# Kernel tuning notes

Measured on AMD Instinct MI355X. Metric: run time of the kernel, lower is better.

## Reference

```python
import jax, jax.numpy as jnp
import numpy as np

E, L = 16384, 2048          # query events, padded history length
N_NODES, N_COMP = 10000, 20  # Poisson base-rate embedding table
T_MAX = 100.0                # time horizon
MEAN_FEAT, VAR_FEAT = 0.5, 0.25


def setup_inputs() -> dict:
    key = jax.random.key(0)
    ks = jax.random.split(key, 7)
    src = jax.random.randint(ks[0], (E,), 0, N_NODES)
    dst = jax.random.randint(ks[1], (E,), 0, N_NODES)
    t = jax.random.uniform(ks[2], (E,), dtype=jnp.float32) * T_MAX
    x_pad = jax.random.normal(ks[3], (E, L), dtype=jnp.float32)
    # histories sorted in time, as event sequences are
    t_pad = jnp.sort(jax.random.uniform(ks[4], (E, L), dtype=jnp.float32) * T_MAX, axis=1)
    # Poisson base-rate params: per-node embeddings, rate = softplus(<e_src, e_dst>)
    emb_src = jax.random.normal(ks[5], (N_NODES, N_COMP), dtype=jnp.float32) * 0.1
    emb_dst = jax.random.normal(ks[6], (N_NODES, N_COMP), dtype=jnp.float32) * 0.1
    # exponential Hawkes kernel params
    alpha = jnp.float32(0.5)
    beta = jnp.float32(1.0)
    return dict(src=src, dst=dst, t=t, x_pad=x_pad, t_pad=t_pad,
                emb_src=emb_src, emb_dst=emb_dst, alpha=alpha, beta=beta)


def reference(src, dst, t, x_pad, t_pad, emb_src, emb_dst, alpha, beta):
    # base_rate(src, dst): Poisson intensity per event pair
    out = jax.nn.softplus(jnp.einsum('ec,ec->e', emb_src[src], emb_dst[dst]))

    # __get_prev_t_mask / __get_last_t_mask: cumsum-based last-event selection
    mask_prev = t_pad < t[:, None]                       # [E, L] bool
    acc = jnp.cumsum(mask_prev.astype(jnp.int32), axis=1)
    ranks = acc.max(axis=1, keepdims=True) - acc
    mask = (ranks < 1) & mask_prev                       # <= one True per row

    is_prev_event = mask.any(axis=1)                     # [E]
    idx = jnp.argmax(mask, axis=1)                       # position of the last prev event
    rows = jnp.arange(t.shape[0])

    # gather last event's feature/time (dummy row 0 where no prev event; masked out below)
    x_last = jax.nn.sigmoid((x_pad[rows, idx] - MEAN_FEAT) / VAR_FEAT)
    t_last = t_pad[rows, idx]

    # Hawkes kernel(src,dst,t_cur,x_last,t_last): alpha * x_last * exp(-beta * dt)
    kval = alpha * x_last * jnp.exp(-beta * (t - t_last))
    incr = jnp.where(is_prev_event, kval, jnp.float32(0.0))
    return (out + incr).astype(jnp.float32)
```

## Files before the change

### kernel.cpp

```cpp
#include <hip/hip_runtime.h>
#include <math.h>

#define NEVENTS 16384
#define LHIST   2048
#define NCOMP   20

__global__ __launch_bounds__(64) void markov_kernel(
        const int*   __restrict__ src,
        const int*   __restrict__ dst,
        const float* __restrict__ t,
        const float* __restrict__ x_pad,
        const float* __restrict__ t_pad,
        const float* __restrict__ emb_src,
        const float* __restrict__ emb_dst,
        const float* __restrict__ alpha_p,
        const float* __restrict__ beta_p,
        float*       __restrict__ out) {
    int e = blockIdx.x * blockDim.x + threadIdx.x;
    if (e >= NEVENTS) return;

    const float alpha = alpha_p[0];
    const float beta  = beta_p[0];

    const int s = src[e];
    const int d = dst[e];
    const float* es = emb_src + (size_t)s * NCOMP;
    const float* ed = emb_dst + (size_t)d * NCOMP;
    float dot = 0.0f;
    #pragma unroll
    for (int c = 0; c < NCOMP; ++c) dot += es[c] * ed[c];
    float sp = fmaxf(dot, 0.0f) + log1pf(expf(-fabsf(dot)));

    const float tq = t[e];
    const float* row = t_pad + (size_t)e * LHIST;
    int lo = 0, hi = LHIST;
    while (lo < hi) {
        int mid = (lo + hi) >> 1;
        if (row[mid] < tq) lo = mid + 1; else hi = mid;
    }
    const int count = lo;

    float incr = 0.0f;
    if (count > 0) {
        const int idx = count - 1;
        const float tl = row[idx];
        const float xv = x_pad[(size_t)e * LHIST + idx];
        const float z  = (xv - 0.5f) * 4.0f;
        const float xs = 1.0f / (1.0f + expf(-z));
        incr = alpha * xs * expf(-beta * (tq - tl));
    }

    out[e] = sp + incr;
}

extern "C" void kernel_launch(void* const* d_in, const int* in_sizes, int n_in,
                              void* d_out, int out_size, void* d_ws, size_t ws_size,
                              hipStream_t stream) {
    const int*   src     = (const int*)  d_in[0];
    const int*   dst     = (const int*)  d_in[1];
    const float* t       = (const float*)d_in[2];
    const float* x_pad   = (const float*)d_in[3];
    const float* t_pad   = (const float*)d_in[4];
    const float* emb_src = (const float*)d_in[5];
    const float* emb_dst = (const float*)d_in[6];
    const float* alpha_p = (const float*)d_in[7];
    const float* beta_p  = (const float*)d_in[8];
    float* out = (float*)d_out;

    dim3 block(64);
    dim3 grid(NEVENTS / 64);
    markov_kernel<<<grid, block, 0, stream>>>(src, dst, t, x_pad, t_pad,
                                              emb_src, emb_dst, alpha_p, beta_p, out);
}
```

Measured before the change: 232.6 us.

## Assign one wavefront per event with ballot-based two-level search

Each event is now handled by a full 64-lane wavefront instead of one thread. The per-thread serial binary search is replaced by a two-level ballot search: 16 lanes sample every 128th element to find the chunk, then the whole wave loads that 128-element chunk as float2 and counts with ballots. The embedding dot product becomes a lane-parallel multiply followed by a shuffle reduction. The goal is to replace eleven dependent, uncoalesced global loads per thread with two coalesced wave loads. The cost is 64 times more threads, while each wave does little work.

```diff
diff --git a/kernel.cpp b/kernel.cpp
--- a/kernel.cpp
+++ b/kernel.cpp
@@ -4,8 +4,9 @@
 #define NEVENTS 16384
 #define LHIST   2048
 #define NCOMP   20
+#define WAVES_PER_BLOCK 4
 
-__global__ __launch_bounds__(64) void markov_kernel(
+__global__ __launch_bounds__(64 * WAVES_PER_BLOCK) void markov_kernel(
         const int*   __restrict__ src,
         const int*   __restrict__ dst,
         const float* __restrict__ t,
@@ -16,41 +17,49 @@
         const float* __restrict__ alpha_p,
         const float* __restrict__ beta_p,
         float*       __restrict__ out) {
-    int e = blockIdx.x * blockDim.x + threadIdx.x;
-    if (e >= NEVENTS) return;
+    const int wid  = blockIdx.x * WAVES_PER_BLOCK + (threadIdx.x >> 6);
+    const int lane = threadIdx.x & 63;
+    if (wid >= NEVENTS) return;
+    const int e = wid;
 
-    const float alpha = alpha_p[0];
-    const float beta  = beta_p[0];
+    const float tq = t[e];
+    const float* row = t_pad + (size_t)e * LHIST;
+
+    const int spos = (lane < 16) ? (lane << 7) : 0;
+    const float sv = row[spos];
+    const unsigned long long b1 = __ballot(sv < tq) & 0xFFFFull;
+    const int j = __popcll(b1) - 1;
+
+    float incr = 0.0f;
+    if (j >= 0) {
+        const float2* c2 = (const float2*)(row + ((size_t)j << 7));
+        const float2 v = c2[lane];
+        const int cin = __popcll(__ballot(v.x < tq)) + __popcll(__ballot(v.y < tq));
+        const int li  = cin - 1;
+        const int idx = (j << 7) + li;
+
+        const float cand = (li & 1) ? v.y : v.x;
+        const float tl   = __shfl(cand, li >> 1);
+
+        const float xv = x_pad[(size_t)e * LHIST + idx];
+        const float z  = (xv - 0.5f) * 4.0f;
+        const float xs = 1.0f / (1.0f + __expf(-z));
+        const float alpha = alpha_p[0];
+        const float beta  = beta_p[0];
+        incr = alpha * xs * __expf(-beta * (tq - tl));
+    }
 
     const int s = src[e];
     const int d = dst[e];
-    const float* es = emb_src + (size_t)s * NCOMP;
-    const float* ed = emb_dst + (size_t)d * NCOMP;
-    float dot = 0.0f;
+    float p = 0.0f;
+    if (lane < NCOMP) {
+        p = emb_src[(size_t)s * NCOMP + lane] * emb_dst[(size_t)d * NCOMP + lane];
+    }
     #pragma unroll
-    for (int c = 0; c < NCOMP; ++c) dot += es[c] * ed[c];
-    float sp = fmaxf(dot, 0.0f) + log1pf(expf(-fabsf(dot)));
+    for (int off = 32; off > 0; off >>= 1) p += __shfl_xor(p, off);
+    const float sp = fmaxf(p, 0.0f) + log1pf(expf(-fabsf(p)));
 
-    const float tq = t[e];
-    const float* row = t_pad + (size_t)e * LHIST;
-    int lo = 0, hi = LHIST;
-    while (lo < hi) {
-        int mid = (lo + hi) >> 1;
-        if (row[mid] < tq) lo = mid + 1; else hi = mid;
-    }
-    const int count = lo;
-
-    float incr = 0.0f;
-    if (count > 0) {
-        const int idx = count - 1;
-        const float tl = row[idx];
-        const float xv = x_pad[(size_t)e * LHIST + idx];
-        const float z  = (xv - 0.5f) * 4.0f;
-        const float xs = 1.0f / (1.0f + expf(-z));
-        incr = alpha * xs * expf(-beta * (tq - tl));
-    }
-
-    out[e] = sp + incr;
+    if (lane == 0) out[e] = sp + incr;
 }
 
 extern "C" void kernel_launch(void* const* d_in, const int* in_sizes, int n_in,
@@ -67,8 +76,7 @@
     const float* beta_p  = (const float*)d_in[8];
     float* out = (float*)d_out;
 
-    dim3 block(64);
-    dim3 grid(NEVENTS / 64);
-    markov_kernel<<<grid, block, 0, stream>>>(src, dst, t, x_pad, t_pad,
-                                              emb_src, emb_dst, alpha_p, beta_p, out);
+    const int blocks = NEVENTS / WAVES_PER_BLOCK;
+    markov_kernel<<<blocks, 64 * WAVES_PER_BLOCK, 0, stream>>>(
+        src, dst, t, x_pad, t_pad, emb_src, emb_dst, alpha_p, beta_p, out);
 }
```

Measured after the change: 261.2 us. +12.3%, slower.
